# Performance work log

Hardware: AMD Instinct MI355X
Metric: run time of the kernel (lower is better)

## Reference

```python
import jax, jax.numpy as jnp
import numpy as np

LN_EPS = 1e-5


def setup_inputs() -> dict:
    N, E, D_IN, D_OUT = 100000, 640000, 128, 128
    key = jax.random.key(0)
    k1, k2, k3 = jax.random.split(key, 3)
    h_in = jax.random.normal(k1, (N, D_IN), dtype=jnp.float32)
    edge_index = jax.random.randint(k2, (2, E), 0, N, dtype=jnp.int64)
    # GCNConv linear weight (PyG stores lin without bias; bias added after aggregation)
    W = jax.random.normal(k3, (D_IN, D_OUT), dtype=jnp.float32) * (1.0 / np.sqrt(D_IN))
    b = jnp.zeros((D_OUT,), dtype=jnp.float32)
    prelu_a = jnp.full((1,), 0.25, dtype=jnp.float32)  # nn.PReLU default init
    gamma = jnp.ones((D_OUT,), dtype=jnp.float32)
    beta = jnp.zeros((D_OUT,), dtype=jnp.float32)
    return {"h_in": h_in, "edge_index": edge_index, "W": W, "b": b,
            "prelu_a": prelu_a, "gamma": gamma, "beta": beta}


def gcn_conv(h_in, edge_index, W, b):
    N = h_in.shape[0]
    x = h_in @ W  # (N, D_out)
    src, dst = edge_index[0], edge_index[1]
    # add self loops (PyG GCNConv default add_self_loops=True, weight 1)
    loop = jnp.arange(N, dtype=src.dtype)
    src_f = jnp.concatenate([src, loop])
    dst_f = jnp.concatenate([dst, loop])
    w_f = jnp.ones(src_f.shape[0], dtype=x.dtype)
    # symmetric normalization: deg^{-1/2}[src] * w * deg^{-1/2}[dst]
    deg = jax.ops.segment_sum(w_f, dst_f, num_segments=N)
    dis = jnp.where(deg > 0, jax.lax.rsqrt(jnp.maximum(deg, 1e-12)), 0.0)
    norm = dis[src_f] * w_f * dis[dst_f]  # (E+N,)
    msgs = norm[:, None] * x[src_f]       # gather + scale
    out = jax.ops.segment_sum(msgs, dst_f, num_segments=N)  # scatter-add
    return out + b


def reference(h_in, edge_index, W, b, prelu_a, gamma, beta):
    h = gcn_conv(h_in, edge_index, W, b)
    # PReLU (single shared slope)
    h = jnp.where(h >= 0, h, prelu_a[0] * h)
    # LayerNorm over last dim
    mu = jnp.mean(h, axis=-1, keepdims=True)
    var = jnp.mean(jnp.square(h - mu), axis=-1, keepdims=True)
    h = (h - mu) * jax.lax.rsqrt(var + LN_EPS) * gamma + beta
    # Dropout: identity in eval mode
    return h
```

## Files before the change

kernel.cpp:

```cpp
#include <hip/hip_runtime.h>
#include <hip/hip_bf16.h>
#include <stdint.h>

#define LNEPS 1e-5f
#define CAP 32

typedef __attribute__((ext_vector_type(4))) float f32x4;
typedef __attribute__((ext_vector_type(8))) short s16x8;

__device__ __forceinline__ float bf_lo(uint32_t packed) {
    union { uint32_t u; float f; } v; v.u = packed << 16; return v.f;
}
__device__ __forceinline__ float bf_hi(uint32_t packed) {
    union { uint32_t u; float f; } v; v.u = packed & 0xffff0000u; return v.f;
}
__device__ __forceinline__ uint16_t f2bf(float x) {
    union { float f; uint32_t u; } v; v.f = x;
    return (uint16_t)((v.u + 0x7fffu + ((v.u >> 16) & 1u)) >> 16);
}
__device__ __forceinline__ uint32_t pack2(float lo, float hi) {
    return (uint32_t)f2bf(lo) | ((uint32_t)f2bf(hi) << 16);
}

__global__ __launch_bounds__(256) void k_detect_zero(const uint32_t* __restrict__ h32,
                                                     const uint32_t* __restrict__ w32,
                                                     const uint32_t* __restrict__ ei32,
                                                     const uint32_t* __restrict__ g32,
                                                     int* __restrict__ flags,
                                                     int* __restrict__ cnt, int N) {
    if (blockIdx.x != 0) {
        int i = (blockIdx.x - 1) * 256 + threadIdx.x;
        if (i < N) cnt[i] = 0;
        return;
    }
    __shared__ int sh_h, sh_w, sh_e;
    if (threadIdx.x == 0) { sh_h = 0; sh_w = 0; sh_e = 0; }
    __syncthreads();
    int ch = 0, cw = 0; uint32_t eo = 0;
    for (int i = threadIdx.x; i < 8192; i += 256) {
        uint32_t ex = (h32[i] >> 7) & 0xFF;
        ch += (ex >= 100 && ex <= 140) ? 1 : 0;
    }
    for (int i = threadIdx.x; i < 4096; i += 256) {
        uint32_t ex = (w32[i] >> 7) & 0xFF;
        cw += (ex >= 90 && ex <= 140) ? 1 : 0;
    }
    for (int i = threadIdx.x; i < 2048; i += 256) {
        eo |= ei32[2 * i + 1];
    }
    atomicAdd(&sh_h, ch);
    atomicAdd(&sh_w, cw);
    atomicOr(&sh_e, (eo != 0u) ? 1 : 0);
    __syncthreads();
    if (threadIdx.x == 0) {
        flags[0] = (sh_h > 5734) ? 1 : 0;
        flags[1] = (sh_w > 2867) ? 1 : 0;
        flags[2] = (sh_e == 0) ? 1 : 0;
        flags[3] = (g32[0] == 0x3F803F80u) ? 1 : 0;
    }
}

__global__ __launch_bounds__(256) void k_fillslot(const void* __restrict__ eiv,
                                                  const int* __restrict__ flags,
                                                  int E, int* __restrict__ cnt,
                                                  int* __restrict__ colslots) {
    int e = blockIdx.x * blockDim.x + threadIdx.x;
    if (e >= E) return;
    int s, d;
    if (flags[2]) {
        const long long* ei = (const long long*)eiv;
        s = (int)ei[e]; d = (int)ei[(size_t)E + e];
    } else {
        const int* ei = (const int*)eiv;
        s = ei[e]; d = ei[E + e];
    }
    int pos = atomicAdd(&cnt[d], 1);
    if (pos < CAP) colslots[(d << 5) + pos] = s;
}

__global__ __launch_bounds__(256) void k_dis_wconv(const int* __restrict__ cnt,
                                                   float* __restrict__ dis,
                                                   const void* __restrict__ Wv,
                                                   const int* __restrict__ flags,
                                                   uint16_t* __restrict__ Wt,
                                                   int N, int db) {
    int b = blockIdx.x;
    if (b < db) {
        int i = b * 256 + threadIdx.x;
        if (i < N) dis[i] = rsqrtf((float)cnt[i] + 1.0f);
        return;
    }
    int widx = (b - db) * 256 + threadIdx.x;
    if (widx < 16384) {
        int n = widx >> 7, k = widx & 127;
        uint16_t v;
        if (flags[1]) v = ((const uint16_t*)Wv)[k * 128 + n];
        else          v = f2bf(((const float*)Wv)[k * 128 + n]);
        Wt[n * 128 + k] = v;
    }
}

__global__ __launch_bounds__(256) void k_gather(const int* __restrict__ cnt,
                                                const int* __restrict__ slots,
                                                const float* __restrict__ dis,
                                                const void* __restrict__ hv,
                                                const int* __restrict__ flags,
                                                uint32_t* __restrict__ agg,
                                                int N) {
    int gid = blockIdx.x * 256 + threadIdx.x;
    int node = gid >> 4;
    if (node >= N) return;
    const int strip = gid & 15;
    int deg0 = cnt[node];
    int deg  = deg0 < CAP ? deg0 : CAP;
    const int4* cb = (const int4*)(slots + (node << 5));
    float a[8] = {0, 0, 0, 0, 0, 0, 0, 0};

    if (flags[0]) {
        const uint4* h4 = (const uint4*)hv;
        for (int base = 0; base < deg; base += 4) {
            int4 c = cb[base >> 2];
            int cols[4] = {c.x, c.y, c.z, c.w};
            int mlim = deg - base;
#pragma unroll
            for (int i = 1; i < 4; ++i) if (i >= mlim) cols[i] = cols[0];
            float dsv[4]; uint4 r[4];
#pragma unroll
            for (int i = 0; i < 4; ++i) dsv[i] = dis[cols[i]];
#pragma unroll
            for (int i = 0; i < 4; ++i) r[i] = h4[(size_t)cols[i] * 16 + strip];
#pragma unroll
            for (int i = 0; i < 4; ++i) {
                if (i < mlim) {
                    float ds = dsv[i];
                    a[0] += ds * bf_lo(r[i].x); a[1] += ds * bf_hi(r[i].x);
                    a[2] += ds * bf_lo(r[i].y); a[3] += ds * bf_hi(r[i].y);
                    a[4] += ds * bf_lo(r[i].z); a[5] += ds * bf_hi(r[i].z);
                    a[6] += ds * bf_lo(r[i].w); a[7] += ds * bf_hi(r[i].w);
                }
            }
        }
        float dn = dis[node];
        uint4 s4 = h4[(size_t)node * 16 + strip];
        float hs[8] = {bf_lo(s4.x), bf_hi(s4.x), bf_lo(s4.y), bf_hi(s4.y),
                       bf_lo(s4.z), bf_hi(s4.z), bf_lo(s4.w), bf_hi(s4.w)};
        uint4 ov;
        ov.x = pack2(dn * a[0] + dn * dn * hs[0], dn * a[1] + dn * dn * hs[1]);
        ov.y = pack2(dn * a[2] + dn * dn * hs[2], dn * a[3] + dn * dn * hs[3]);
        ov.z = pack2(dn * a[4] + dn * dn * hs[4], dn * a[5] + dn * dn * hs[5]);
        ov.w = pack2(dn * a[6] + dn * dn * hs[6], dn * a[7] + dn * dn * hs[7]);
        ((uint4*)agg)[(size_t)node * 16 + strip] = ov;
    } else {
        const float4* h8 = (const float4*)hv;
        for (int base = 0; base < deg; base += 4) {
            int4 c = cb[base >> 2];
            int cols[4] = {c.x, c.y, c.z, c.w};
            int mlim = deg - base;
#pragma unroll
            for (int i = 1; i < 4; ++i) if (i >= mlim) cols[i] = cols[0];
            float dsv[4]; float4 ra[4], rb[4];
#pragma unroll
            for (int i = 0; i < 4; ++i) dsv[i] = dis[cols[i]];
#pragma unroll
            for (int i = 0; i < 4; ++i) {
                const float4* rp = h8 + (size_t)cols[i] * 32 + strip * 2;
                ra[i] = rp[0];
                rb[i] = rp[1];
            }
#pragma unroll
            for (int i = 0; i < 4; ++i) {
                if (i < mlim) {
                    float ds = dsv[i];
                    a[0] += ds * ra[i].x; a[1] += ds * ra[i].y;
                    a[2] += ds * ra[i].z; a[3] += ds * ra[i].w;
                    a[4] += ds * rb[i].x; a[5] += ds * rb[i].y;
                    a[6] += ds * rb[i].z; a[7] += ds * rb[i].w;
                }
            }
        }
        float dn = dis[node];
        const float4* sp = h8 + (size_t)node * 32 + strip * 2;
        float4 s0 = sp[0], s1 = sp[1];
        uint4 ov;
        ov.x = pack2(dn * a[0] + dn * dn * s0.x, dn * a[1] + dn * dn * s0.y);
        ov.y = pack2(dn * a[2] + dn * dn * s0.z, dn * a[3] + dn * dn * s0.w);
        ov.z = pack2(dn * a[4] + dn * dn * s1.x, dn * a[5] + dn * dn * s1.y);
        ov.w = pack2(dn * a[6] + dn * dn * s1.z, dn * a[7] + dn * dn * s1.w);
        ((uint4*)agg)[(size_t)node * 16 + strip] = ov;
    }
}

#define ASTR 136
__global__ __launch_bounds__(256) void k_gemm_ln(const uint16_t* __restrict__ agg,
                                                 const uint16_t* __restrict__ Wt,
                                                 const void* __restrict__ biasv,
                                                 const void* __restrict__ pav,
                                                 const void* __restrict__ gammav,
                                                 const void* __restrict__ betav,
                                                 float* __restrict__ out,
                                                 const int* __restrict__ flags,
                                                 int N) {
    __shared__ uint16_t As[128 * ASTR];
    __shared__ uint16_t Bs[128 * ASTR];

    const int t    = threadIdx.x;
    const int lane = t & 63;
    const int w    = t >> 6;
    const int q    = lane >> 4;
    const int nl   = lane & 15;
    const int m0   = blockIdx.x * 128;
    const int f_s  = flags[3];

    float a_slope, bcv[8], gcv[8], bev[8];
    if (f_s) {
        a_slope = bf_lo((uint32_t)((const uint16_t*)pav)[0]);
#pragma unroll
        for (int ct = 0; ct < 8; ++ct) {
            int cc = ct * 16 + nl;
            bcv[ct] = bf_lo((uint32_t)((const uint16_t*)biasv)[cc]);
            gcv[ct] = bf_lo((uint32_t)((const uint16_t*)gammav)[cc]);
            bev[ct] = bf_lo((uint32_t)((const uint16_t*)betav)[cc]);
        }
    } else {
        a_slope = ((const float*)pav)[0];
#pragma unroll
        for (int ct = 0; ct < 8; ++ct) {
            int cc = ct * 16 + nl;
            bcv[ct] = ((const float*)biasv)[cc];
            gcv[ct] = ((const float*)gammav)[cc];
            bev[ct] = ((const float*)betav)[cc];
        }
    }

    {
        int r  = t >> 1;
        int sg = t & 1;
        const uint4 zero = make_uint4(0, 0, 0, 0);
        int grow = m0 + r;
        const uint4* pa4 = (const uint4*)(agg + (size_t)grow * 128 + sg * 64);
        uint4* da = (uint4*)&As[r * ASTR + sg * 64];
#pragma unroll
        for (int u = 0; u < 8; ++u) da[u] = (grow < N) ? pa4[u] : zero;
        const uint4* pb4 = (const uint4*)(Wt + (size_t)r * 128 + sg * 64);
        uint4* db = (uint4*)&Bs[r * ASTR + sg * 64];
#pragma unroll
        for (int u = 0; u < 8; ++u) db[u] = pb4[u];
    }
    __syncthreads();

    f32x4 acc[2][8];
#pragma unroll
    for (int rt = 0; rt < 2; ++rt)
#pragma unroll
        for (int ct = 0; ct < 8; ++ct) acc[rt][ct] = (f32x4){0.f, 0.f, 0.f, 0.f};

#pragma unroll
    for (int kk = 0; kk < 128; kk += 32) {
        s16x8 af[2], bfr[8];
#pragma unroll
        for (int rt = 0; rt < 2; ++rt)
            af[rt] = *(const s16x8*)&As[(w * 32 + rt * 16 + nl) * ASTR + kk + q * 8];
#pragma unroll
        for (int ct = 0; ct < 8; ++ct)
            bfr[ct] = *(const s16x8*)&Bs[(ct * 16 + nl) * ASTR + kk + q * 8];
#pragma unroll
        for (int rt = 0; rt < 2; ++rt)
#pragma unroll
            for (int ct = 0; ct < 8; ++ct)
                acc[rt][ct] = __builtin_amdgcn_mfma_f32_16x16x32_bf16(
                    af[rt], bfr[ct], acc[rt][ct], 0, 0, 0);
    }

#pragma unroll
    for (int rt = 0; rt < 2; ++rt) {
#pragma unroll
        for (int reg = 0; reg < 4; ++reg) {
            float z[8];
            float s1 = 0.0f, s2 = 0.0f;
#pragma unroll
            for (int ct = 0; ct < 8; ++ct) {
                float y = acc[rt][ct][reg] + bcv[ct];
                y = (y >= 0.0f) ? y : a_slope * y;
                z[ct] = y;
                s1 += y; s2 += y * y;
            }
#pragma unroll
            for (int m = 8; m >= 1; m >>= 1) {
                s1 += __shfl_xor(s1, m);
                s2 += __shfl_xor(s2, m);
            }
            float mu  = s1 * (1.0f / 128.0f);
            float var = s2 * (1.0f / 128.0f) - mu * mu;
            float rs  = rsqrtf(fmaxf(var, 0.0f) + LNEPS);
            int grow = m0 + w * 32 + rt * 16 + q * 4 + reg;
            if (grow < N) {
                float* op = out + (size_t)grow * 128;
#pragma unroll
                for (int ct = 0; ct < 8; ++ct)
                    op[ct * 16 + nl] = (z[ct] - mu) * rs * gcv[ct] + bev[ct];
            }
        }
    }
}

extern "C" void kernel_launch(void* const* d_in, const int* in_sizes, int n_in,
                              void* d_out, int out_size, void* d_ws, size_t ws_size,
                              hipStream_t stream) {
    const int N = in_sizes[0] / 128;
    const int E = in_sizes[1] / 2;

    const void* h     = d_in[0];
    const void* ei    = d_in[1];
    const void* W     = d_in[2];
    const void* bias  = d_in[3];
    const void* pa    = d_in[4];
    const void* gamma = d_in[5];
    const void* beta  = d_in[6];
    float* out = (float*)d_out;

    uint32_t* agg    = (uint32_t*)d_ws;
    int*      slots  = (int*)(agg + (size_t)N * 64);
    int*      cnt    = slots + (size_t)N * CAP;
    float*    dis    = (float*)(cnt + N);
    uint16_t* Wt     = (uint16_t*)(dis + N);
    int*      flags  = (int*)(Wt + 16384);

    const int zb = (N + 255) / 256;
    k_detect_zero<<<1 + zb, 256, 0, stream>>>((const uint32_t*)h, (const uint32_t*)W,
                                              (const uint32_t*)ei, (const uint32_t*)gamma,
                                              flags, cnt, N);
    k_fillslot<<<(E + 255) / 256, 256, 0, stream>>>(ei, flags, E, cnt, slots);

    const int db = (N + 255) / 256;
    k_dis_wconv<<<db + 64, 256, 0, stream>>>(cnt, dis, W, flags, Wt, N, db);

    const int gb = (N * 16 + 255) / 256;
    k_gather<<<gb, 256, 0, stream>>>(cnt, slots, dis, h, flags, agg, N);

    const int mblocks = (N + 127) / 128;
    k_gemm_ln<<<mblocks, 256, 0, stream>>>((const uint16_t*)agg, Wt, bias, pa,
                                           gamma, beta, out, flags, N);
}
```

Baseline: 236.4 us.

## Drop dis kernel, compute degree rsqrt inline in gather, fold W conversion into fillslot

Removes the separate kernel that computed per-node deg^-1/2 and converted W. The W transpose/convert is moved into extra blocks of the edge-fill kernel, and the gather now computes rsqrt from cnt directly instead of reading a precomputed dis array. The bf16 gather path also unrolls to 8 neighbors per iteration for more memory-level parallelism. This saves one launch and one pass over N, at the cost of redundant rsqrt work per edge and higher register pressure.

```diff
diff --git a/kernel.cpp b/kernel.cpp
--- a/kernel.cpp
+++ b/kernel.cpp
@@ -63,8 +63,23 @@
 __global__ __launch_bounds__(256) void k_fillslot(const void* __restrict__ eiv,
                                                   const int* __restrict__ flags,
                                                   int E, int* __restrict__ cnt,
-                                                  int* __restrict__ colslots) {
-    int e = blockIdx.x * blockDim.x + threadIdx.x;
+                                                  int* __restrict__ colslots,
+                                                  const void* __restrict__ Wv,
+                                                  uint16_t* __restrict__ Wt,
+                                                  int eb) {
+    int b = blockIdx.x;
+    if (b >= eb) {
+        int widx = (b - eb) * 256 + threadIdx.x;
+        if (widx < 16384) {
+            int n = widx >> 7, k = widx & 127;
+            uint16_t v;
+            if (flags[1]) v = ((const uint16_t*)Wv)[k * 128 + n];
+            else          v = f2bf(((const float*)Wv)[k * 128 + n]);
+            Wt[n * 128 + k] = v;
+        }
+        return;
+    }
+    int e = b * blockDim.x + threadIdx.x;
     if (e >= E) return;
     int s, d;
     if (flags[2]) {
@@ -78,31 +93,8 @@
     if (pos < CAP) colslots[(d << 5) + pos] = s;
 }
 
-__global__ __launch_bounds__(256) void k_dis_wconv(const int* __restrict__ cnt,
-                                                   float* __restrict__ dis,
-                                                   const void* __restrict__ Wv,
-                                                   const int* __restrict__ flags,
-                                                   uint16_t* __restrict__ Wt,
-                                                   int N, int db) {
-    int b = blockIdx.x;
-    if (b < db) {
-        int i = b * 256 + threadIdx.x;
-        if (i < N) dis[i] = rsqrtf((float)cnt[i] + 1.0f);
-        return;
-    }
-    int widx = (b - db) * 256 + threadIdx.x;
-    if (widx < 16384) {
-        int n = widx >> 7, k = widx & 127;
-        uint16_t v;
-        if (flags[1]) v = ((const uint16_t*)Wv)[k * 128 + n];
-        else          v = f2bf(((const float*)Wv)[k * 128 + n]);
-        Wt[n * 128 + k] = v;
-    }
-}
-
 __global__ __launch_bounds__(256) void k_gather(const int* __restrict__ cnt,
                                                 const int* __restrict__ slots,
-                                                const float* __restrict__ dis,
                                                 const void* __restrict__ hv,
                                                 const int* __restrict__ flags,
                                                 uint32_t* __restrict__ agg,
@@ -113,26 +105,28 @@
     const int strip = gid & 15;
     int deg0 = cnt[node];
     int deg  = deg0 < CAP ? deg0 : CAP;
+    float dn = rsqrtf((float)deg0 + 1.0f);
     const int4* cb = (const int4*)(slots + (node << 5));
     float a[8] = {0, 0, 0, 0, 0, 0, 0, 0};
 
     if (flags[0]) {
         const uint4* h4 = (const uint4*)hv;
-        for (int base = 0; base < deg; base += 4) {
-            int4 c = cb[base >> 2];
-            int cols[4] = {c.x, c.y, c.z, c.w};
+        for (int base = 0; base < deg; base += 8) {
+            int4 c0 = cb[base >> 2];
+            int4 c1 = cb[(base >> 2) + 1];
+            int cols[8] = {c0.x, c0.y, c0.z, c0.w, c1.x, c1.y, c1.z, c1.w};
             int mlim = deg - base;
 #pragma unroll
-            for (int i = 1; i < 4; ++i) if (i >= mlim) cols[i] = cols[0];
-            float dsv[4]; uint4 r[4];
-#pragma unroll
-            for (int i = 0; i < 4; ++i) dsv[i] = dis[cols[i]];
-#pragma unroll
-            for (int i = 0; i < 4; ++i) r[i] = h4[(size_t)cols[i] * 16 + strip];
-#pragma unroll
-            for (int i = 0; i < 4; ++i) {
+            for (int i = 1; i < 8; ++i) if (i >= mlim) cols[i] = cols[0];
+            float cv[8]; uint4 r[8];
+#pragma unroll
+            for (int i = 0; i < 8; ++i) cv[i] = (float)cnt[cols[i]];
+#pragma unroll
+            for (int i = 0; i < 8; ++i) r[i] = h4[(size_t)cols[i] * 16 + strip];
+#pragma unroll
+            for (int i = 0; i < 8; ++i) {
                 if (i < mlim) {
-                    float ds = dsv[i];
+                    float ds = rsqrtf(cv[i] + 1.0f);
                     a[0] += ds * bf_lo(r[i].x); a[1] += ds * bf_hi(r[i].x);
                     a[2] += ds * bf_lo(r[i].y); a[3] += ds * bf_hi(r[i].y);
                     a[4] += ds * bf_lo(r[i].z); a[5] += ds * bf_hi(r[i].z);
@@ -140,7 +134,6 @@
                 }
             }
         }
-        float dn = dis[node];
         uint4 s4 = h4[(size_t)node * 16 + strip];
         float hs[8] = {bf_lo(s4.x), bf_hi(s4.x), bf_lo(s4.y), bf_hi(s4.y),
                        bf_lo(s4.z), bf_hi(s4.z), bf_lo(s4.w), bf_hi(s4.w)};
@@ -158,9 +151,9 @@
             int mlim = deg - base;
 #pragma unroll
             for (int i = 1; i < 4; ++i) if (i >= mlim) cols[i] = cols[0];
-            float dsv[4]; float4 ra[4], rb[4];
-#pragma unroll
-            for (int i = 0; i < 4; ++i) dsv[i] = dis[cols[i]];
+            float cv[4]; float4 ra[4], rb[4];
+#pragma unroll
+            for (int i = 0; i < 4; ++i) cv[i] = (float)cnt[cols[i]];
 #pragma unroll
             for (int i = 0; i < 4; ++i) {
                 const float4* rp = h8 + (size_t)cols[i] * 32 + strip * 2;
@@ -170,7 +163,7 @@
 #pragma unroll
             for (int i = 0; i < 4; ++i) {
                 if (i < mlim) {
-                    float ds = dsv[i];
+                    float ds = rsqrtf(cv[i] + 1.0f);
                     a[0] += ds * ra[i].x; a[1] += ds * ra[i].y;
                     a[2] += ds * ra[i].z; a[3] += ds * ra[i].w;
                     a[4] += ds * rb[i].x; a[5] += ds * rb[i].y;
@@ -178,7 +171,6 @@
                 }
             }
         }
-        float dn = dis[node];
         const float4* sp = h8 + (size_t)node * 32 + strip * 2;
         float4 s0 = sp[0], s1 = sp[1];
         uint4 ov;
@@ -321,21 +313,19 @@
     uint32_t* agg    = (uint32_t*)d_ws;
     int*      slots  = (int*)(agg + (size_t)N * 64);
     int*      cnt    = slots + (size_t)N * CAP;
-    float*    dis    = (float*)(cnt + N);
-    uint16_t* Wt     = (uint16_t*)(dis + N);
+    uint16_t* Wt     = (uint16_t*)(cnt + N);
     int*      flags  = (int*)(Wt + 16384);
 
     const int zb = (N + 255) / 256;
     k_detect_zero<<<1 + zb, 256, 0, stream>>>((const uint32_t*)h, (const uint32_t*)W,
                                               (const uint32_t*)ei, (const uint32_t*)gamma,
                                               flags, cnt, N);
-    k_fillslot<<<(E + 255) / 256, 256, 0, stream>>>(ei, flags, E, cnt, slots);
-
-    const int db = (N + 255) / 256;
-    k_dis_wconv<<<db + 64, 256, 0, stream>>>(cnt, dis, W, flags, Wt, N, db);
+
+    const int eb = (E + 255) / 256;
+    k_fillslot<<<eb + 64, 256, 0, stream>>>(ei, flags, E, cnt, slots, W, Wt, eb);
 
     const int gb = (N * 16 + 255) / 256;
-    k_gather<<<gb, 256, 0, stream>>>(cnt, slots, dis, h, flags, agg, N);
+    k_gather<<<gb, 256, 0, stream>>>(cnt, slots, h, flags, agg, N);
 
     const int mblocks = (N + 127) / 128;
     k_gemm_ln<<<mblocks, 256, 0, stream>>>((const uint16_t*)agg, Wt, bias, pa,
```

After: 233.1 us. No clear change (-1.4%).
